# Performance work log

Measured on AMD Instinct MI355X. Metric: run time of the kernel, lower is better.

Reference implementation:

```python
import jax, jax.numpy as jnp
import numpy as np

NQ, NL, NPCA, NCLS = 7, 6, 32, 3129
DIM = 2 ** NQ
B = 8192

# PauliZ diagonal per wire (PennyLane convention: wire 0 = most significant bit)
_bits = (np.arange(DIM)[None, :] >> (NQ - 1 - np.arange(NQ))[:, None]) & 1
Z_DIAG = jnp.asarray(1.0 - 2.0 * _bits, dtype=jnp.float32)  # (NQ, DIM)

# CNOT(control=q, target=(q+1)%NQ) as a static basis-index permutation (involution)
def _cnot_perm(c, t):
    idx = np.arange(DIM)
    cbit = (idx >> (NQ - 1 - c)) & 1
    return jnp.asarray(idx ^ (cbit << (NQ - 1 - t)))
CNOT_PERMS = [_cnot_perm(q, (q + 1) % NQ) for q in range(NQ)]

def _apply_ry(state, q, theta):
    # state: (B, DIM) complex64; theta: (B,) per-sample or scalar
    st = state.reshape(-1, 2 ** q, 2, 2 ** (NQ - 1 - q))
    th = jnp.asarray(theta)
    c = jnp.cos(th / 2)
    s = jnp.sin(th / 2)
    if th.ndim == 1:
        c = c[:, None, None]
        s = s[:, None, None]
    a0, a1 = st[:, :, 0, :], st[:, :, 1, :]
    return jnp.stack((c * a0 - s * a1, s * a0 + c * a1), axis=2).reshape(-1, DIM)

def _apply_rz(state, q, theta):
    # RZ = diag(e^{-i t/2}, e^{+i t/2}); theta is a shared scalar here
    st = state.reshape(-1, 2 ** q, 2, 2 ** (NQ - 1 - q))
    p = jnp.exp(jnp.complex64(-0.5j) * theta)
    a0, a1 = st[:, :, 0, :], st[:, :, 1, :]
    return jnp.stack((p * a0, jnp.conj(p) * a1), axis=2).reshape(-1, DIM)

def _quantum_circuit(feats, weights):
    # feats: (B, NL*NQ) encoding angles (data re-uploading); weights: (NL, NQ, 2)
    bsz = feats.shape[0]
    state = jnp.zeros((bsz, DIM), jnp.complex64).at[:, 0].set(1.0)
    for layer in range(NL):
        for q in range(NQ):
            # RY data-encoding followed by variational RY rotate about the same axis -> fuse angles
            state = _apply_ry(state, q, feats[:, layer * NQ + q] + weights[layer, q, 0])
            state = _apply_rz(state, q, weights[layer, q, 1])
        for q in range(NQ):  # ring entanglement
            state = state[:, CNOT_PERMS[q]]
    probs = state.real ** 2 + state.imag ** 2  # (B, DIM)
    return probs @ Z_DIAG.T  # (B, NQ) <Z_i> expectation values

def setup_inputs() -> dict:
    key = jax.random.key(0)
    ks = jax.random.split(key, 8)
    def lin(k, i, o):
        return (jax.random.normal(k, (i, o), jnp.float32) / np.sqrt(i)).astype(jnp.float32)
    return {
        "x": jax.random.normal(ks[0], (B, NPCA), jnp.float32),
        "feature_scale": jnp.ones((NPCA,), jnp.float32),
        "quantum_weights": jax.random.normal(ks[1], (NL, NQ, 2), jnp.float32) * 0.1,
        "qh_w1": lin(ks[2], NQ, 64), "qh_b1": jnp.zeros((64,), jnp.float32),
        "qh_w2": lin(ks[3], 64, NCLS), "qh_b2": jnp.zeros((NCLS,), jnp.float32),
        "ch_w1": lin(ks[4], NPCA, 256), "ch_b1": jnp.zeros((256,), jnp.float32),
        "ch_w2": lin(ks[5], 256, 128), "ch_b2": jnp.zeros((128,), jnp.float32),
        "ch_w3": lin(ks[6], 128, NCLS), "ch_b3": jnp.zeros((NCLS,), jnp.float32),
    }

def reference(x, feature_scale, quantum_weights, qh_w1, qh_b1, qh_w2, qh_b2,
              ch_w1, ch_b1, ch_w2, ch_b2, ch_w3, ch_b3):
    # prepare_features: learned scale -> arctan squash -> zero-pad to NL*NQ angles
    feats = jnp.arctan(x * feature_scale)
    feats = jnp.pad(feats, ((0, 0), (0, NL * NQ - NPCA)))
    q_features = _quantum_circuit(feats, quantum_weights)          # (B, NQ)
    q_logits = jax.nn.relu(q_features @ qh_w1 + qh_b1) @ qh_w2 + qh_b2
    h = jax.nn.relu(x @ ch_w1 + ch_b1)                             # dropout = identity at eval
    h = jax.nn.relu(h @ ch_w2 + ch_b2)
    c_logits = h @ ch_w3 + ch_b3
    return (q_logits, c_logits, q_features)
```

## Files before the change

### kernel.cpp

```cpp
#include <hip/hip_runtime.h>
#include <hip/hip_bf16.h>
#include <math.h>

#define NQ 7
#define NL 6
#define BATCH 8192
#define NPCA 32
#define NCLS 3129
#define NGATE 42

typedef __attribute__((ext_vector_type(8))) short short8;
typedef __attribute__((ext_vector_type(4))) float f32x4;

__device__ __forceinline__ void gload_lds16(const void* g, void* l) {
    __builtin_amdgcn_global_load_lds(
        (const __attribute__((address_space(1))) void*)g,
        (__attribute__((address_space(3))) void*)l, 16, 0, 0);
}

__global__ __launch_bounds__(256) void quantum_kernel(
    const float* __restrict__ x,
    const float* __restrict__ fscale,
    const float* __restrict__ qw,
    const float* __restrict__ qh_w1,
    const float* __restrict__ qh_b1,
    float* __restrict__ qf_out,
    __hip_bfloat16* __restrict__ hq_out)
{
    __shared__ float pzc[NGATE], pzs[NGATE], w0s[NGATE];
    int tid = threadIdx.x;
    if (tid < NGATE) {
        float t = qw[tid * 2 + 1] * 0.5f;
        float s, c;
        sincosf(t, &s, &c);
        pzs[tid] = s; pzc[tid] = c;
        w0s[tid] = qw[tid * 2 + 0];
    }
    __syncthreads();

    const int lane = tid & 63;
    const int wave = tid >> 6;
    const int sample = blockIdx.x * 4 + wave;

    float myfeat = 0.f;
    if (lane < NPCA) myfeat = atanf(x[sample * NPCA + lane] * fscale[lane]);

    float s0r = (lane == 0) ? 1.f : 0.f, s0i = 0.f, s1r = 0.f, s1i = 0.f;

    for (int layer = 0; layer < NL; ++layer) {
        for (int q = 0; q < NQ; ++q) {
            const int g = layer * NQ + q;
            const int b = NQ - 1 - q;
            float fv = (g < NPCA) ? __shfl(myfeat, g) : 0.f;
            float th = (fv + w0s[g]) * 0.5f;
            float s = __sinf(th), c = __cosf(th);
            if (b == 0) {
                float n0r = c * s0r - s * s1r, n0i = c * s0i - s * s1i;
                float n1r = s * s0r + c * s1r, n1i = s * s0i + c * s1i;
                s0r = n0r; s0i = n0i; s1r = n1r; s1i = n1i;
            } else {
                int m = 1 << (b - 1);
                float p0r = __shfl_xor(s0r, m), p0i = __shfl_xor(s0i, m);
                float p1r = __shfl_xor(s1r, m), p1i = __shfl_xor(s1i, m);
                if (((lane >> (b - 1)) & 1) == 0) {
                    s0r = c * s0r - s * p0r; s0i = c * s0i - s * p0i;
                    s1r = c * s1r - s * p1r; s1i = c * s1i - s * p1i;
                } else {
                    s0r = s * p0r + c * s0r; s0i = s * p0i + c * s0i;
                    s1r = s * p1r + c * s1r; s1i = s * p1i + c * s1i;
                }
            }
            float pc = pzc[g], ps = pzs[g];
            if (b == 0) {
                float t0 = pc * s0r + ps * s0i; s0i = pc * s0i - ps * s0r; s0r = t0;
                float t1 = pc * s1r - ps * s1i; s1i = pc * s1i + ps * s1r; s1r = t1;
            } else {
                float e = (((lane >> (b - 1)) & 1) == 0) ? ps : -ps;
                float t0 = pc * s0r + e * s0i; s0i = pc * s0i - e * s0r; s0r = t0;
                float t1 = pc * s1r + e * s1i; s1i = pc * s1i - e * s1r; s1r = t1;
            }
        }
        #pragma unroll
        for (int cq = 0; cq < NQ; ++cq) {
            if (cq == NQ - 1) {
                float r = __shfl_xor(s1r, 32), im = __shfl_xor(s1i, 32);
                s1r = r; s1i = im;
            } else if (cq == NQ - 2) {
                if (lane & 1) {
                    float tr = s0r; s0r = s1r; s1r = tr;
                    float ti = s0i; s0i = s1i; s1i = ti;
                }
            } else {
                const int bc = NQ - 1 - cq;
                const int bt = bc - 1;
                int m = 1 << (bt - 1);
                float p0r = __shfl_xor(s0r, m), p0i = __shfl_xor(s0i, m);
                float p1r = __shfl_xor(s1r, m), p1i = __shfl_xor(s1i, m);
                if ((lane >> (bc - 1)) & 1) {
                    s0r = p0r; s0i = p0i; s1r = p1r; s1i = p1i;
                }
            }
        }
    }

    float p0 = s0r * s0r + s0i * s0i;
    float p1 = s1r * s1r + s1i * s1i;
    float psum = p0 + p1;
    float qf[7];
    #pragma unroll
    for (int k = 0; k < 6; ++k)
        qf[k] = (((lane >> (5 - k)) & 1) ? -psum : psum);
    qf[6] = p0 - p1;
    #pragma unroll
    for (int off = 32; off >= 1; off >>= 1) {
        #pragma unroll
        for (int k = 0; k < 7; ++k) qf[k] += __shfl_xor(qf[k], off);
    }

    float acc = qh_b1[lane];
    #pragma unroll
    for (int k = 0; k < 7; ++k) acc += qf[k] * qh_w1[k * 64 + lane];
    hq_out[sample * 64 + lane] = __float2bfloat16(fmaxf(acc, 0.f));
    if (lane < 7) qf_out[sample * 7 + lane] = qf[lane];
}

__global__ __launch_bounds__(256) void chead_kernel(
    const float* __restrict__ x,
    const float* __restrict__ w1,
    const float* __restrict__ b1,
    const float* __restrict__ w2,
    const float* __restrict__ b2,
    __hip_bfloat16* __restrict__ h2out)
{
    __shared__ float xs[16][33];
    __shared__ float h1s[16][260];
    const int tid = threadIdx.x;
    const int row0 = blockIdx.x * 16;

    for (int i = tid; i < 16 * 32; i += 256) {
        int r = i >> 5, k = i & 31;
        xs[r][k] = x[(row0 + r) * 32 + k];
    }
    __syncthreads();

    {
        float w1c[32];
        #pragma unroll
        for (int k = 0; k < 32; ++k) w1c[k] = w1[k * 256 + tid];
        float bb = b1[tid];
        #pragma unroll
        for (int r = 0; r < 16; ++r) {
            float a = bb;
            #pragma unroll
            for (int k = 0; k < 32; ++k) a += xs[r][k] * w1c[k];
            h1s[r][tid] = fmaxf(a, 0.f);
        }
    }
    __syncthreads();

    {
        const int c0 = (tid & 31) * 4;
        const int r0 = (tid >> 5) * 2;
        float4 bv = *(const float4*)&b2[c0];
        float a0[4] = {bv.x, bv.y, bv.z, bv.w};
        float a1[4] = {bv.x, bv.y, bv.z, bv.w};
        for (int k = 0; k < 256; k += 4) {
            float4 h0 = *(const float4*)&h1s[r0][k];
            float4 h1 = *(const float4*)&h1s[r0 + 1][k];
            #pragma unroll
            for (int j = 0; j < 4; ++j) {
                float4 w = *(const float4*)&w2[(size_t)(k + j) * 128 + c0];
                float hv0 = (j == 0) ? h0.x : (j == 1) ? h0.y : (j == 2) ? h0.z : h0.w;
                float hv1 = (j == 0) ? h1.x : (j == 1) ? h1.y : (j == 2) ? h1.z : h1.w;
                a0[0] += hv0 * w.x; a0[1] += hv0 * w.y; a0[2] += hv0 * w.z; a0[3] += hv0 * w.w;
                a1[0] += hv1 * w.x; a1[1] += hv1 * w.y; a1[2] += hv1 * w.z; a1[3] += hv1 * w.w;
            }
        }
        #pragma unroll
        for (int rr = 0; rr < 2; ++rr) {
            float* a = rr ? a1 : a0;
            __hip_bfloat162 q0, q1;
            q0.x = __float2bfloat16(fmaxf(a[0], 0.f));
            q0.y = __float2bfloat16(fmaxf(a[1], 0.f));
            q1.x = __float2bfloat16(fmaxf(a[2], 0.f));
            q1.y = __float2bfloat16(fmaxf(a[3], 0.f));
            size_t base = (size_t)(row0 + r0 + rr) * 128 + c0;
            *(__hip_bfloat162*)&h2out[base]     = q0;
            *(__hip_bfloat162*)&h2out[base + 2] = q1;
        }
    }
}

__global__ __launch_bounds__(256) void transpose_cast2(
    const float* __restrict__ Wq, __hip_bfloat16* __restrict__ Wqt,
    const float* __restrict__ Wc, __hip_bfloat16* __restrict__ Wct, int N)
{
    __shared__ float tile[64][65];
    const int tid = threadIdx.x;
    const int n0 = blockIdx.x * 64;
    const float* W; __hip_bfloat16* Wt; int K, k0;
    if (blockIdx.y == 0) { W = Wq; Wt = Wqt; K = 64;  k0 = 0; }
    else                 { W = Wc; Wt = Wct; K = 128; k0 = (blockIdx.y - 1) * 64; }

    #pragma unroll
    for (int i = 0; i < 16; ++i) {
        int id = tid + i * 256;
        int kr = id >> 6, nc = id & 63;
        int n = n0 + nc;
        tile[kr][nc] = (n < N) ? W[(size_t)(k0 + kr) * N + n] : 0.f;
    }
    __syncthreads();
    #pragma unroll
    for (int i = 0; i < 16; ++i) {
        int id = tid + i * 256;
        int nr = id >> 6, kc = id & 63;
        int n = n0 + nr;
        if (n < N) Wt[(size_t)n * K + k0 + kc] = __float2bfloat16(tile[kc][nr]);
    }
}

__global__ __launch_bounds__(256) void gemm_mfma_dual(
    const __hip_bfloat16* __restrict__ A0, const __hip_bfloat16* __restrict__ B0,
    const float* __restrict__ bias0, float* __restrict__ C0,
    const __hip_bfloat16* __restrict__ A1, const __hip_bfloat16* __restrict__ B1,
    const float* __restrict__ bias1, float* __restrict__ C1, int N)
{
    __shared__ alignas(16) unsigned char shraw[32768];
    __hip_bfloat16* Alds = (__hip_bfloat16*)shraw;
    __hip_bfloat16* Blds = Alds + 128 * 64;
    float* scr = (float*)shraw;

    const int z = blockIdx.z;
    const __hip_bfloat16* A  = z ? A1 : A0;
    const __hip_bfloat16* Bt = z ? B1 : B0;
    const float* bias        = z ? bias1 : bias0;
    float* C                 = z ? C1 : C0;
    const int K              = z ? 128 : 64;

    const int tid  = threadIdx.x;
    const int lane = tid & 63;
    const int wave = tid >> 6;
    const int wr = wave >> 1, wc = wave & 1;
    const int row0 = blockIdx.y * 128;
    const int col0 = blockIdx.x * 128;

    f32x4 acc[4][4] = {};

    for (int kb = 0; kb < K; kb += 64) {
        #pragma unroll
        for (int i = 0; i < 4; ++i) {
            int id = tid + i * 256;
            int r = id >> 3;
            int c = id & 7;
            int cs = c ^ (r & 7);
            gload_lds16(&A[(size_t)(row0 + r) * K + kb + cs * 8], &Alds[id * 8]);
        }
        #pragma unroll
        for (int i = 0; i < 4; ++i) {
            int id = tid + i * 256;
            int r = id >> 3;
            int c = id & 7;
            int cs = c ^ (r & 7);
            int n = col0 + r;
            if (n >= N) n = N - 1;
            gload_lds16(&Bt[(size_t)n * K + kb + cs * 8], &Blds[id * 8]);
        }
        __syncthreads();

        const int frow = lane & 15;
        const int chi  = lane >> 4;
        #pragma unroll
        for (int kk = 0; kk < 2; ++kk) {
            short8 af[4], bf[4];
            #pragma unroll
            for (int m = 0; m < 4; ++m) {
                int r = wr * 64 + m * 16 + frow;
                int cs = (kk * 4 + chi) ^ (r & 7);
                af[m] = *(const short8*)&Alds[r * 64 + cs * 8];
            }
            #pragma unroll
            for (int n = 0; n < 4; ++n) {
                int r = wc * 64 + n * 16 + frow;
                int cs = (kk * 4 + chi) ^ (r & 7);
                bf[n] = *(const short8*)&Blds[r * 64 + cs * 8];
            }
            #pragma unroll
            for (int m = 0; m < 4; ++m)
                #pragma unroll
                for (int n = 0; n < 4; ++n)
                    acc[m][n] = __builtin_amdgcn_mfma_f32_16x16x32_bf16(
                        af[m], bf[n], acc[m][n], 0, 0, 0);
        }
        __syncthreads();
    }

    const int g = lane >> 4;
    const int fcol = lane & 15;
    const int ccr = tid & 127;
    const int bc  = col0 + ccr;
    const float bv = (bc < N) ? bias[bc] : 0.f;

    #pragma unroll
    for (int p = 0; p < 2; ++p) {
        if (p) __syncthreads();
        #pragma unroll
        for (int mm = 0; mm < 2; ++mm) {
            #pragma unroll
            for (int n = 0; n < 4; ++n) {
                int rl = wr * 32 + mm * 16 + g * 4;
                int cc = wc * 64 + n * 16 + fcol;
                int ccs = cc ^ (((rl >> 2) & 1) << 4);
                #pragma unroll
                for (int r = 0; r < 4; ++r)
                    scr[(rl + r) * 128 + ccs] = acc[2 * p + mm][n][r];
            }
        }
        __syncthreads();
        if (bc < N) {
            #pragma unroll
            for (int i = 0; i < 32; ++i) {
                int id = i * 256 + tid;
                int rl = id >> 7;
                int ccs = ccr ^ (((rl >> 2) & 1) << 4);
                int grow = row0 + p * 32 + ((rl >> 5) << 6) + (rl & 31);
                C[(size_t)grow * N + bc] = scr[rl * 128 + ccs] + bv;
            }
        }
    }
}

extern "C" void kernel_launch(void* const* d_in, const int* in_sizes, int n_in,
                              void* d_out, int out_size, void* d_ws, size_t ws_size,
                              hipStream_t stream)
{
    const float* x   = (const float*)d_in[0];
    const float* fs  = (const float*)d_in[1];
    const float* qw  = (const float*)d_in[2];
    const float* qw1 = (const float*)d_in[3];
    const float* qb1 = (const float*)d_in[4];
    const float* qw2 = (const float*)d_in[5];
    const float* qb2 = (const float*)d_in[6];
    const float* cw1 = (const float*)d_in[7];
    const float* cb1 = (const float*)d_in[8];
    const float* cw2 = (const float*)d_in[9];
    const float* cb2 = (const float*)d_in[10];
    const float* cw3 = (const float*)d_in[11];
    const float* cb3 = (const float*)d_in[12];

    float* q_logits = (float*)d_out;
    float* c_logits = q_logits + (size_t)BATCH * NCLS;
    float* qf_out   = c_logits + (size_t)BATCH * NCLS;

    const int NPAD = 3200;
    __hip_bfloat16* hq   = (__hip_bfloat16*)d_ws;
    __hip_bfloat16* h2   = hq + (size_t)BATCH * 64;
    __hip_bfloat16* qw2t = h2 + (size_t)BATCH * 128;
    __hip_bfloat16* cw3t = qw2t + (size_t)NPAD * 64;

    dim3 tg((NCLS + 63) / 64, 3);
    transpose_cast2<<<tg, 256, 0, stream>>>(qw2, qw2t, cw3, cw3t, NCLS);

    quantum_kernel<<<BATCH / 4, 256, 0, stream>>>(x, fs, qw, qw1, qb1, qf_out, hq);
    chead_kernel<<<BATCH / 16, 256, 0, stream>>>(x, cw1, cb1, cw2, cb2, h2);

    dim3 grid((NCLS + 127) / 128, BATCH / 128, 2);
    gemm_mfma_dual<<<grid, 256, 0, stream>>>(hq, qw2t, qb2, q_logits,
                                             h2, cw3t, cb3, c_logits, NCLS);
}
```

Baseline: 115.1 us.

## Merge prep kernels into one launch, fuse CNOT ring, precompute RY angles, nontemporal stores

Combines the quantum-circuit, classical-head and weight-transpose kernels into a single launch whose work is chosen by block index, removing two launch gaps and letting the three jobs run side by side. Inside the quantum path, each lane computes one gate's RY sin/cos up front and the others fetch it with a shuffle, instead of every lane doing transcendentals per gate. The seven sequential CNOT permutations are replaced by one composed permutation built from a few shuffles. The GEMM epilogue writes its large logit outputs with nontemporal stores to reduce cache pollution. In exchange, register pressure and LDS size are now set by the largest branch for every block.

New measurement: 143.0 us. +24.2%, slower.

```diff
diff --git a/kernel.cpp b/kernel.cpp
--- a/kernel.cpp
+++ b/kernel.cpp
@@ -9,6 +9,11 @@
 #define NCLS 3129
 #define NGATE 42
 
+#define NBQ 2048
+#define NBC 512
+#define NBX 49
+#define NBT (3 * NBX)
+
 typedef __attribute__((ext_vector_type(8))) short short8;
 typedef __attribute__((ext_vector_type(4))) float f32x4;
 
@@ -18,204 +23,199 @@
         (__attribute__((address_space(3))) void*)l, 16, 0, 0);
 }
 
-__global__ __launch_bounds__(256) void quantum_kernel(
+__global__ __launch_bounds__(256) void prep_kernel(
     const float* __restrict__ x,
     const float* __restrict__ fscale,
     const float* __restrict__ qw,
     const float* __restrict__ qh_w1,
     const float* __restrict__ qh_b1,
+    const float* __restrict__ cw1, const float* __restrict__ cb1,
+    const float* __restrict__ cw2, const float* __restrict__ cb2,
+    const float* __restrict__ qw2, const float* __restrict__ cw3,
     float* __restrict__ qf_out,
-    __hip_bfloat16* __restrict__ hq_out)
+    __hip_bfloat16* __restrict__ hq_out,
+    __hip_bfloat16* __restrict__ h2_out,
+    __hip_bfloat16* __restrict__ qw2t,
+    __hip_bfloat16* __restrict__ cw3t)
 {
-    __shared__ float pzc[NGATE], pzs[NGATE], w0s[NGATE];
-    int tid = threadIdx.x;
-    if (tid < NGATE) {
-        float t = qw[tid * 2 + 1] * 0.5f;
-        float s, c;
-        sincosf(t, &s, &c);
-        pzs[tid] = s; pzc[tid] = c;
-        w0s[tid] = qw[tid * 2 + 0];
-    }
-    __syncthreads();
-
-    const int lane = tid & 63;
-    const int wave = tid >> 6;
-    const int sample = blockIdx.x * 4 + wave;
-
-    float myfeat = 0.f;
-    if (lane < NPCA) myfeat = atanf(x[sample * NPCA + lane] * fscale[lane]);
-
-    float s0r = (lane == 0) ? 1.f : 0.f, s0i = 0.f, s1r = 0.f, s1i = 0.f;
-
-    for (int layer = 0; layer < NL; ++layer) {
-        for (int q = 0; q < NQ; ++q) {
-            const int g = layer * NQ + q;
-            const int b = NQ - 1 - q;
-            float fv = (g < NPCA) ? __shfl(myfeat, g) : 0.f;
-            float th = (fv + w0s[g]) * 0.5f;
-            float s = __sinf(th), c = __cosf(th);
-            if (b == 0) {
-                float n0r = c * s0r - s * s1r, n0i = c * s0i - s * s1i;
-                float n1r = s * s0r + c * s1r, n1i = s * s0i + c * s1i;
-                s0r = n0r; s0i = n0i; s1r = n1r; s1i = n1i;
-            } else {
-                int m = 1 << (b - 1);
-                float p0r = __shfl_xor(s0r, m), p0i = __shfl_xor(s0i, m);
-                float p1r = __shfl_xor(s1r, m), p1i = __shfl_xor(s1i, m);
-                if (((lane >> (b - 1)) & 1) == 0) {
-                    s0r = c * s0r - s * p0r; s0i = c * s0i - s * p0i;
-                    s1r = c * s1r - s * p1r; s1i = c * s1i - s * p1i;
+    __shared__ alignas(16) unsigned char smem[18752];
+    const int bid = blockIdx.x;
+    const int tid = threadIdx.x;
+
+    if (bid < NBQ) {
+        float* pzc = (float*)smem;
+        float* pzs = pzc + NGATE;
+        float* w0s = pzs + NGATE;
+        if (tid < NGATE) {
+            float t = qw[tid * 2 + 1] * 0.5f;
+            float s, c;
+            sincosf(t, &s, &c);
+            pzs[tid] = s; pzc[tid] = c;
+            w0s[tid] = qw[tid * 2 + 0];
+        }
+        __syncthreads();
+
+        const int lane = tid & 63;
+        const int wave = tid >> 6;
+        const int sample = bid * 4 + wave;
+
+        float myfeat = 0.f;
+        if (lane < NPCA) myfeat = atanf(x[sample * NPCA + lane] * fscale[lane]);
+
+        float sv = 0.f, cv = 1.f;
+        if (lane < NGATE) {
+            float th = (((lane < NPCA) ? myfeat : 0.f) + w0s[lane]) * 0.5f;
+            sv = __sinf(th); cv = __cosf(th);
+        }
+
+        const int t0 = (lane ^ (lane >> 1)) & 63;
+        const int t1 = t0 ^ 48;
+        const bool odd = (lane & 1) != 0;
+
+        float s0r = (lane == 0) ? 1.f : 0.f, s0i = 0.f, s1r = 0.f, s1i = 0.f;
+
+        for (int layer = 0; layer < NL; ++layer) {
+            #pragma unroll
+            for (int q = 0; q < NQ; ++q) {
+                const int g = layer * NQ + q;
+                const int b = NQ - 1 - q;
+                float s = __shfl(sv, g), c = __shfl(cv, g);
+                if (b == 0) {
+                    float n0r = c * s0r - s * s1r, n0i = c * s0i - s * s1i;
+                    float n1r = s * s0r + c * s1r, n1i = s * s0i + c * s1i;
+                    s0r = n0r; s0i = n0i; s1r = n1r; s1i = n1i;
                 } else {
-                    s0r = s * p0r + c * s0r; s0i = s * p0i + c * s0i;
-                    s1r = s * p1r + c * s1r; s1i = s * p1i + c * s1i;
+                    int m = 1 << (b - 1);
+                    float p0r = __shfl_xor(s0r, m), p0i = __shfl_xor(s0i, m);
+                    float p1r = __shfl_xor(s1r, m), p1i = __shfl_xor(s1i, m);
+                    if (((lane >> (b - 1)) & 1) == 0) {
+                        s0r = c * s0r - s * p0r; s0i = c * s0i - s * p0i;
+                        s1r = c * s1r - s * p1r; s1i = c * s1i - s * p1i;
+                    } else {
+                        s0r = s * p0r + c * s0r; s0i = s * p0i + c * s0i;
+                        s1r = s * p1r + c * s1r; s1i = s * p1i + c * s1i;
+                    }
                 }
-            }
-            float pc = pzc[g], ps = pzs[g];
-            if (b == 0) {
-                float t0 = pc * s0r + ps * s0i; s0i = pc * s0i - ps * s0r; s0r = t0;
-                float t1 = pc * s1r - ps * s1i; s1i = pc * s1i + ps * s1r; s1r = t1;
-            } else {
-                float e = (((lane >> (b - 1)) & 1) == 0) ? ps : -ps;
-                float t0 = pc * s0r + e * s0i; s0i = pc * s0i - e * s0r; s0r = t0;
-                float t1 = pc * s1r + e * s1i; s1i = pc * s1i - e * s1r; s1r = t1;
-            }
-        }
-        #pragma unroll
-        for (int cq = 0; cq < NQ; ++cq) {
-            if (cq == NQ - 1) {
-                float r = __shfl_xor(s1r, 32), im = __shfl_xor(s1i, 32);
-                s1r = r; s1i = im;
-            } else if (cq == NQ - 2) {
-                if (lane & 1) {
-                    float tr = s0r; s0r = s1r; s1r = tr;
-                    float ti = s0i; s0i = s1i; s1i = ti;
+                float pc = pzc[g], ps = pzs[g];
+                if (b == 0) {
+                    float u0 = pc * s0r + ps * s0i; s0i = pc * s0i - ps * s0r; s0r = u0;
+                    float u1 = pc * s1r - ps * s1i; s1i = pc * s1i + ps * s1r; s1r = u1;
+                } else {
+                    float e = (((lane >> (b - 1)) & 1) == 0) ? ps : -ps;
+                    float u0 = pc * s0r + e * s0i; s0i = pc * s0i - e * s0r; s0r = u0;
+                    float u1 = pc * s1r + e * s1i; s1i = pc * s1i - e * s1r; s1r = u1;
                 }
-            } else {
-                const int bc = NQ - 1 - cq;
-                const int bt = bc - 1;
-                int m = 1 << (bt - 1);
-                float p0r = __shfl_xor(s0r, m), p0i = __shfl_xor(s0i, m);
-                float p1r = __shfl_xor(s1r, m), p1i = __shfl_xor(s1i, m);
-                if ((lane >> (bc - 1)) & 1) {
-                    s0r = p0r; s0i = p0i; s1r = p1r; s1i = p1i;
+            }
+            float a0r = __shfl(s0r, t0), a0i = __shfl(s0i, t0);
+            float a1r = __shfl(s1r, t0), a1i = __shfl(s1i, t0);
+            float b0r = __shfl(s0r, t1), b0i = __shfl(s0i, t1);
+            float b1r = __shfl(s1r, t1), b1i = __shfl(s1i, t1);
+            s0r = odd ? a1r : a0r;  s0i = odd ? a1i : a0i;
+            s1r = odd ? b0r : b1r;  s1i = odd ? b0i : b1i;
+        }
+
+        float p0 = s0r * s0r + s0i * s0i;
+        float p1 = s1r * s1r + s1i * s1i;
+        float psum = p0 + p1;
+        float qf[7];
+        #pragma unroll
+        for (int k = 0; k < 6; ++k)
+            qf[k] = (((lane >> (5 - k)) & 1) ? -psum : psum);
+        qf[6] = p0 - p1;
+        #pragma unroll
+        for (int off = 32; off >= 1; off >>= 1) {
+            #pragma unroll
+            for (int k = 0; k < 7; ++k) qf[k] += __shfl_xor(qf[k], off);
+        }
+
+        float acc = qh_b1[lane];
+        #pragma unroll
+        for (int k = 0; k < 7; ++k) acc += qf[k] * qh_w1[k * 64 + lane];
+        hq_out[sample * 64 + lane] = __float2bfloat16(fmaxf(acc, 0.f));
+        if (lane < 7) qf_out[sample * 7 + lane] = qf[lane];
+
+    } else if (bid < NBQ + NBC) {
+        float (*xs)[33]   = (float(*)[33])smem;
+        float (*h1s)[260] = (float(*)[260])(smem + 2112);
+        const int row0 = (bid - NBQ) * 16;
+
+        for (int i = tid; i < 16 * 32; i += 256) {
+            int r = i >> 5, k = i & 31;
+            xs[r][k] = x[(row0 + r) * 32 + k];
+        }
+        __syncthreads();
+
+        {
+            float w1c[32];
+            #pragma unroll
+            for (int k = 0; k < 32; ++k) w1c[k] = cw1[k * 256 + tid];
+            float bb = cb1[tid];
+            #pragma unroll
+            for (int r = 0; r < 16; ++r) {
+                float a = bb;
+                #pragma unroll
+                for (int k = 0; k < 32; ++k) a += xs[r][k] * w1c[k];
+                h1s[r][tid] = fmaxf(a, 0.f);
+            }
+        }
+        __syncthreads();
+
+        {
+            const int c0 = (tid & 31) * 4;
+            const int r0 = (tid >> 5) * 2;
+            float4 bv = *(const float4*)&cb2[c0];
+            float a0[4] = {bv.x, bv.y, bv.z, bv.w};
+            float a1[4] = {bv.x, bv.y, bv.z, bv.w};
+            for (int k = 0; k < 256; k += 4) {
+                float4 h0 = *(const float4*)&h1s[r0][k];
+                float4 h1 = *(const float4*)&h1s[r0 + 1][k];
+                #pragma unroll
+                for (int j = 0; j < 4; ++j) {
+                    float4 w = *(const float4*)&cw2[(size_t)(k + j) * 128 + c0];
+                    float hv0 = (j == 0) ? h0.x : (j == 1) ? h0.y : (j == 2) ? h0.z : h0.w;
+                    float hv1 = (j == 0) ? h1.x : (j == 1) ? h1.y : (j == 2) ? h1.z : h1.w;
+                    a0[0] += hv0 * w.x; a0[1] += hv0 * w.y; a0[2] += hv0 * w.z; a0[3] += hv0 * w.w;
+                    a1[0] += hv1 * w.x; a1[1] += hv1 * w.y; a1[2] += hv1 * w.z; a1[3] += hv1 * w.w;
                 }
             }
-        }
-    }
-
-    float p0 = s0r * s0r + s0i * s0i;
-    float p1 = s1r * s1r + s1i * s1i;
-    float psum = p0 + p1;
-    float qf[7];
-    #pragma unroll
-    for (int k = 0; k < 6; ++k)
-        qf[k] = (((lane >> (5 - k)) & 1) ? -psum : psum);
-    qf[6] = p0 - p1;
-    #pragma unroll
-    for (int off = 32; off >= 1; off >>= 1) {
-        #pragma unroll
-        for (int k = 0; k < 7; ++k) qf[k] += __shfl_xor(qf[k], off);
-    }
-
-    float acc = qh_b1[lane];
-    #pragma unroll
-    for (int k = 0; k < 7; ++k) acc += qf[k] * qh_w1[k * 64 + lane];
-    hq_out[sample * 64 + lane] = __float2bfloat16(fmaxf(acc, 0.f));
-    if (lane < 7) qf_out[sample * 7 + lane] = qf[lane];
-}
-
-__global__ __launch_bounds__(256) void chead_kernel(
-    const float* __restrict__ x,
-    const float* __restrict__ w1,
-    const float* __restrict__ b1,
-    const float* __restrict__ w2,
-    const float* __restrict__ b2,
-    __hip_bfloat16* __restrict__ h2out)
-{
-    __shared__ float xs[16][33];
-    __shared__ float h1s[16][260];
-    const int tid = threadIdx.x;
-    const int row0 = blockIdx.x * 16;
-
-    for (int i = tid; i < 16 * 32; i += 256) {
-        int r = i >> 5, k = i & 31;
-        xs[r][k] = x[(row0 + r) * 32 + k];
-    }
-    __syncthreads();
-
-    {
-        float w1c[32];
-        #pragma unroll
-        for (int k = 0; k < 32; ++k) w1c[k] = w1[k * 256 + tid];
-        float bb = b1[tid];
-        #pragma unroll
-        for (int r = 0; r < 16; ++r) {
-            float a = bb;
-            #pragma unroll
-            for (int k = 0; k < 32; ++k) a += xs[r][k] * w1c[k];
-            h1s[r][tid] = fmaxf(a, 0.f);
-        }
-    }
-    __syncthreads();
-
-    {
-        const int c0 = (tid & 31) * 4;
-        const int r0 = (tid >> 5) * 2;
-        float4 bv = *(const float4*)&b2[c0];
-        float a0[4] = {bv.x, bv.y, bv.z, bv.w};
-        float a1[4] = {bv.x, bv.y, bv.z, bv.w};
-        for (int k = 0; k < 256; k += 4) {
-            float4 h0 = *(const float4*)&h1s[r0][k];
-            float4 h1 = *(const float4*)&h1s[r0 + 1][k];
-            #pragma unroll
-            for (int j = 0; j < 4; ++j) {
-                float4 w = *(const float4*)&w2[(size_t)(k + j) * 128 + c0];
-                float hv0 = (j == 0) ? h0.x : (j == 1) ? h0.y : (j == 2) ? h0.z : h0.w;
-                float hv1 = (j == 0) ? h1.x : (j == 1) ? h1.y : (j == 2) ? h1.z : h1.w;
-                a0[0] += hv0 * w.x; a0[1] += hv0 * w.y; a0[2] += hv0 * w.z; a0[3] += hv0 * w.w;
-                a1[0] += hv1 * w.x; a1[1] += hv1 * w.y; a1[2] += hv1 * w.z; a1[3] += hv1 * w.w;
-            }
-        }
-        #pragma unroll
-        for (int rr = 0; rr < 2; ++rr) {
-            float* a = rr ? a1 : a0;
-            __hip_bfloat162 q0, q1;
-            q0.x = __float2bfloat16(fmaxf(a[0], 0.f));
-            q0.y = __float2bfloat16(fmaxf(a[1], 0.f));
-            q1.x = __float2bfloat16(fmaxf(a[2], 0.f));
-            q1.y = __float2bfloat16(fmaxf(a[3], 0.f));
-            size_t base = (size_t)(row0 + r0 + rr) * 128 + c0;
-            *(__hip_bfloat162*)&h2out[base]     = q0;
-            *(__hip_bfloat162*)&h2out[base + 2] = q1;
-        }
-    }
-}
-
-__global__ __launch_bounds__(256) void transpose_cast2(
-    const float* __restrict__ Wq, __hip_bfloat16* __restrict__ Wqt,
-    const float* __restrict__ Wc, __hip_bfloat16* __restrict__ Wct, int N)
-{
-    __shared__ float tile[64][65];
-    const int tid = threadIdx.x;
-    const int n0 = blockIdx.x * 64;
-    const float* W; __hip_bfloat16* Wt; int K, k0;
-    if (blockIdx.y == 0) { W = Wq; Wt = Wqt; K = 64;  k0 = 0; }
-    else                 { W = Wc; Wt = Wct; K = 128; k0 = (blockIdx.y - 1) * 64; }
-
-    #pragma unroll
-    for (int i = 0; i < 16; ++i) {
-        int id = tid + i * 256;
-        int kr = id >> 6, nc = id & 63;
-        int n = n0 + nc;
-        tile[kr][nc] = (n < N) ? W[(size_t)(k0 + kr) * N + n] : 0.f;
-    }
-    __syncthreads();
-    #pragma unroll
-    for (int i = 0; i < 16; ++i) {
-        int id = tid + i * 256;
-        int nr = id >> 6, kc = id & 63;
-        int n = n0 + nr;
-        if (n < N) Wt[(size_t)n * K + k0 + kc] = __float2bfloat16(tile[kc][nr]);
+            #pragma unroll
+            for (int rr = 0; rr < 2; ++rr) {
+                float* a = rr ? a1 : a0;
+                __hip_bfloat162 q0, q1;
+                q0.x = __float2bfloat16(fmaxf(a[0], 0.f));
+                q0.y = __float2bfloat16(fmaxf(a[1], 0.f));
+                q1.x = __float2bfloat16(fmaxf(a[2], 0.f));
+                q1.y = __float2bfloat16(fmaxf(a[3], 0.f));
+                size_t base = (size_t)(row0 + r0 + rr) * 128 + c0;
+                *(__hip_bfloat162*)&h2_out[base]     = q0;
+                *(__hip_bfloat162*)&h2_out[base + 2] = q1;
+            }
+        }
+
+    } else {
+        float (*tile)[65] = (float(*)[65])smem;
+        const int t = bid - (NBQ + NBC);
+        const int y = t / NBX;
+        const int n0 = (t % NBX) * 64;
+        const float* W; __hip_bfloat16* Wt; int K, k0;
+        if (y == 0) { W = qw2; Wt = qw2t; K = 64;  k0 = 0; }
+        else        { W = cw3; Wt = cw3t; K = 128; k0 = (y - 1) * 64; }
+
+        #pragma unroll
+        for (int i = 0; i < 16; ++i) {
+            int id = tid + i * 256;
+            int kr = id >> 6, nc = id & 63;
+            int n = n0 + nc;
+            tile[kr][nc] = (n < NCLS) ? W[(size_t)(k0 + kr) * NCLS + n] : 0.f;
+        }
+        __syncthreads();
+        #pragma unroll
+        for (int i = 0; i < 16; ++i) {
+            int id = tid + i * 256;
+            int nr = id >> 6, kc = id & 63;
+            int n = n0 + nr;
+            if (n < NCLS) Wt[(size_t)n * K + k0 + kc] = __float2bfloat16(tile[kc][nr]);
+        }
     }
 }
 
@@ -323,7 +323,8 @@
                 int rl = id >> 7;
                 int ccs = ccr ^ (((rl >> 2) & 1) << 4);
                 int grow = row0 + p * 32 + ((rl >> 5) << 6) + (rl & 31);
-                C[(size_t)grow * N + bc] = scr[rl * 128 + ccs] + bv;
+                __builtin_nontemporal_store(scr[rl * 128 + ccs] + bv,
+                                            &C[(size_t)grow * N + bc]);
             }
         }
     }
@@ -357,11 +358,9 @@
     __hip_bfloat16* qw2t = h2 + (size_t)BATCH * 128;
     __hip_bfloat16* cw3t = qw2t + (size_t)NPAD * 64;
 
-    dim3 tg((NCLS + 63) / 64, 3);
-    transpose_cast2<<<tg, 256, 0, stream>>>(qw2, qw2t, cw3, cw3t, NCLS);
-
-    quantum_kernel<<<BATCH / 4, 256, 0, stream>>>(x, fs, qw, qw1, qb1, qf_out, hq);
-    chead_kernel<<<BATCH / 16, 256, 0, stream>>>(x, cw1, cb1, cw2, cb2, h2);
+    prep_kernel<<<NBQ + NBC + NBT, 256, 0, stream>>>(
+        x, fs, qw, qw1, qb1, cw1, cb1, cw2, cb2, qw2, cw3,
+        qf_out, hq, h2, qw2t, cw3t);
 
     dim3 grid((NCLS + 127) / 128, BATCH / 128, 2);
     gemm_mfma_dual<<<grid, 256, 0, stream>>>(hq, qw2t, qb2, q_logits,
```
